# Optimization experiments

Measured on AMD Instinct MI355X. Metric: run time of the kernel, lower is better.

Reference implementation:

```python
import jax, jax.numpy as jnp
import numpy as np

EMBED_DIM = 128
NUM_HEADS = 4
HEAD_DIM = EMBED_DIM // NUM_HEADS
B, S = 2, 1024


def setup_inputs() -> dict:
    key = jax.random.key(0)
    ks = jax.random.split(key, 9)
    sc = 1.0 / np.sqrt(EMBED_DIM)
    x = jax.random.normal(ks[0], (B, S, EMBED_DIM), dtype=jnp.float32)
    # torch nn.Linear weights: (out_features, in_features)
    Wq = jax.random.uniform(ks[1], (EMBED_DIM, EMBED_DIM), jnp.float32, -sc, sc)
    bq = jax.random.uniform(ks[2], (EMBED_DIM,), jnp.float32, -sc, sc)
    Wk = jax.random.uniform(ks[3], (EMBED_DIM, EMBED_DIM), jnp.float32, -sc, sc)
    bk = jax.random.uniform(ks[4], (EMBED_DIM,), jnp.float32, -sc, sc)
    Wv = jax.random.uniform(ks[5], (EMBED_DIM, EMBED_DIM), jnp.float32, -sc, sc)
    bv = jax.random.uniform(ks[6], (EMBED_DIM,), jnp.float32, -sc, sc)
    Wo = jax.random.uniform(ks[7], (EMBED_DIM, EMBED_DIM), jnp.float32, -sc, sc)
    bo = jax.random.uniform(ks[8], (EMBED_DIM,), jnp.float32, -sc, sc)
    return {"x": x, "Wq": Wq, "bq": bq, "Wk": Wk, "bk": bk,
            "Wv": Wv, "bv": bv, "Wo": Wo, "bo": bo}


def _heads(y):
    # (B,S,E) -> (B,H,S,D)
    return y.reshape(B, S, NUM_HEADS, HEAD_DIM).transpose(0, 2, 1, 3)


def reference(x, Wq, bq, Wk, bk, Wv, bv, Wo, bo):
    q = _heads(x @ Wq.T + bq)  # (B,H,S,D)
    k = _heads(x @ Wk.T + bk)
    v = _heads(x @ Wv.T + bv)
    # ultrametric (Chebyshev / max-abs) distance: (B,H,S,S)
    dist = jnp.max(jnp.abs(q[:, :, :, None, :] - k[:, :, None, :, :]), axis=-1)
    attn = jax.nn.softmax(-dist, axis=-1)
    attended = jnp.einsum('bhst,bhtd->bhsd', attn, v)
    attended = attended.transpose(0, 2, 1, 3).reshape(B, S, EMBED_DIM)
    return attended @ Wo.T + bo
```

## Files before the change

kernel.cpp:

```cpp
#include <hip/hip_runtime.h>
#include <hip/hip_bf16.h>

#define B_ 2
#define S_ 1024
#define E_ 128
#define H_ 4
#define D_ 32
#define BHSD (B_ * H_ * S_ * D_)
#define LOG2E 1.44269504088896f

__global__ __launch_bounds__(128) void qkv_kernel(
    const float* __restrict__ x,
    const float* __restrict__ Wq, const float* __restrict__ bq,
    const float* __restrict__ Wk, const float* __restrict__ bk,
    const float* __restrict__ Wv, const float* __restrict__ bv,
    float* __restrict__ ws) {
  const int mat = blockIdx.y;
  const float* W    = (mat == 0) ? Wq : (mat == 1) ? Wk : Wv;
  const float* bias = (mat == 0) ? bq : (mat == 1) ? bk : bv;
  const float scale = (mat == 2) ? 1.0f : LOG2E;
  float* outbase = ws + (size_t)mat * BHSD;

  const int row0 = blockIdx.x * 8;
  const int t = threadIdx.x;

  __shared__ __align__(16) float xs[8 * E_];
  const float4* xg = (const float4*)(x + (size_t)row0 * E_);
  float4* xs4 = (float4*)xs;
  #pragma unroll
  for (int i = 0; i < 2; ++i) xs4[t + i * 128] = xg[t + i * 128];
  __syncthreads();

  const int col = t;
  const float4* W4 = (const float4*)(W + (size_t)col * E_);

  float acc[8];
  #pragma unroll
  for (int r = 0; r < 8; ++r) acc[r] = 0.f;

  #pragma unroll 4
  for (int c4 = 0; c4 < E_ / 4; ++c4) {
    float4 w = W4[c4];
    #pragma unroll
    for (int r = 0; r < 8; ++r) {
      float4 xv = xs4[r * (E_ / 4) + c4];
      acc[r] += xv.x * w.x + xv.y * w.y + xv.z * w.z + xv.w * w.w;
    }
  }

  const float bcol = bias[col];
  const int h = col >> 5, d = col & 31;
  #pragma unroll
  for (int r = 0; r < 8; ++r) {
    int row = row0 + r;
    int b = row >> 10, s = row & 1023;
    outbase[(((size_t)(b * H_ + h)) * S_ + s) * D_ + d] = (acc[r] + bcol) * scale;
  }
}

#define QSTRIDE 36
#define PSTRIDE 68

__global__ __launch_bounds__(256) void attn_kernel(
    const float* __restrict__ qg, const float* __restrict__ kg_,
    const float* __restrict__ vg,
    float* __restrict__ part_o, float* __restrict__ part_l) {
  __shared__ __align__(16) float Qs[64 * QSTRIDE];
  __shared__ __align__(16) float Ks[64 * QSTRIDE];
  __shared__ __align__(16) float Vs[64 * QSTRIDE];
  __shared__ __align__(16) float Ps[64 * PSTRIDE];

  const int bx = blockIdx.x;
  const int kc  = bx & 3;
  const int rtl = (bx >> 2) & 15;
  const int head = bx >> 6;
  const int t = threadIdx.x;
  const int w = t >> 6;
  const int lane = t & 63;
  const int rg = lane >> 3;
  const int kg = lane & 7;

  const float* qbase = qg  + (size_t)head * S_ * D_ + (size_t)rtl * 64 * D_;
  const float* kbase = kg_ + (size_t)head * S_ * D_ + (size_t)kc * 256 * D_;
  const float* vbase = vg  + (size_t)head * S_ * D_ + (size_t)kc * 256 * D_;

  {
    const float4* src = (const float4*)qbase;
    #pragma unroll
    for (int i = 0; i < 2; ++i) {
      int f = t + i * 256;
      int r = f >> 3, c4 = f & 7;
      *(float4*)(Qs + r * QSTRIDE + c4 * 4) = src[f];
    }
  }

  float O[8][4];
  #pragma unroll
  for (int i = 0; i < 8; ++i)
    #pragma unroll
    for (int c = 0; c < 4; ++c) O[i][c] = 0.f;
  float lrow[8];
  #pragma unroll
  for (int i = 0; i < 8; ++i) lrow[i] = 0.f;

  for (int it = 0; it < 4; ++it) {
    {
      const float4* ksrc = (const float4*)(kbase + (size_t)it * 64 * D_);
      const float4* vsrc = (const float4*)(vbase + (size_t)it * 64 * D_);
      #pragma unroll
      for (int i = 0; i < 2; ++i) {
        int f = t + i * 256;
        int r = f >> 3, c4 = f & 7;
        *(float4*)(Ks + r * QSTRIDE + c4 * 4) = ksrc[f];
        *(float4*)(Vs + r * QSTRIDE + c4 * 4) = vsrc[f];
      }
    }
    __syncthreads();

    float dist[8][2];
    #pragma unroll
    for (int i = 0; i < 8; ++i) { dist[i][0] = 0.f; dist[i][1] = 0.f; }

    #pragma unroll 2
    for (int c = 0; c < 8; ++c) {
      float4 qv[8];
      #pragma unroll
      for (int i = 0; i < 8; ++i)
        qv[i] = *(const float4*)(Qs + (rg + 8 * i) * QSTRIDE + c * 4);
      float4 kv[2];
      #pragma unroll
      for (int j = 0; j < 2; ++j)
        kv[j] = *(const float4*)(Ks + (w * 16 + kg + 8 * j) * QSTRIDE + c * 4);
      #pragma unroll
      for (int i = 0; i < 8; ++i) {
        #pragma unroll
        for (int j = 0; j < 2; ++j) {
          float m0 = fmaxf(fabsf(qv[i].x - kv[j].x), fabsf(qv[i].y - kv[j].y));
          float m1 = fmaxf(fabsf(qv[i].z - kv[j].z), fabsf(qv[i].w - kv[j].w));
          dist[i][j] = fmaxf(dist[i][j], fmaxf(m0, m1));
        }
      }
    }

    float pp[8][2];
    #pragma unroll
    for (int i = 0; i < 8; ++i) {
      #pragma unroll
      for (int j = 0; j < 2; ++j) {
        float p = exp2f(-dist[i][j]);
        pp[i][j] = p;
        lrow[i] += p;
      }
    }
    #pragma unroll
    for (int j = 0; j < 2; ++j) {
      float* dst = Ps + (w * 16 + kg + 8 * j) * PSTRIDE + rg * 8;
      *(float4*)(dst + 0) = make_float4(pp[0][j], pp[1][j], pp[2][j], pp[3][j]);
      *(float4*)(dst + 4) = make_float4(pp[4][j], pp[5][j], pp[6][j], pp[7][j]);
    }
    __syncthreads();

    const int tk0 = w * 16;
    #pragma unroll 4
    for (int u = 0; u < 16; ++u) {
      const int tk = tk0 + u;
      float4 pa = *(const float4*)(Ps + tk * PSTRIDE + rg * 8);
      float4 pb = *(const float4*)(Ps + tk * PSTRIDE + rg * 8 + 4);
      float4 vv = *(const float4*)(Vs + tk * QSTRIDE + kg * 4);
      O[0][0] = fmaf(pa.x, vv.x, O[0][0]); O[0][1] = fmaf(pa.x, vv.y, O[0][1]);
      O[0][2] = fmaf(pa.x, vv.z, O[0][2]); O[0][3] = fmaf(pa.x, vv.w, O[0][3]);
      O[1][0] = fmaf(pa.y, vv.x, O[1][0]); O[1][1] = fmaf(pa.y, vv.y, O[1][1]);
      O[1][2] = fmaf(pa.y, vv.z, O[1][2]); O[1][3] = fmaf(pa.y, vv.w, O[1][3]);
      O[2][0] = fmaf(pa.z, vv.x, O[2][0]); O[2][1] = fmaf(pa.z, vv.y, O[2][1]);
      O[2][2] = fmaf(pa.z, vv.z, O[2][2]); O[2][3] = fmaf(pa.z, vv.w, O[2][3]);
      O[3][0] = fmaf(pa.w, vv.x, O[3][0]); O[3][1] = fmaf(pa.w, vv.y, O[3][1]);
      O[3][2] = fmaf(pa.w, vv.z, O[3][2]); O[3][3] = fmaf(pa.w, vv.w, O[3][3]);
      O[4][0] = fmaf(pb.x, vv.x, O[4][0]); O[4][1] = fmaf(pb.x, vv.y, O[4][1]);
      O[4][2] = fmaf(pb.x, vv.z, O[4][2]); O[4][3] = fmaf(pb.x, vv.w, O[4][3]);
      O[5][0] = fmaf(pb.y, vv.x, O[5][0]); O[5][1] = fmaf(pb.y, vv.y, O[5][1]);
      O[5][2] = fmaf(pb.y, vv.z, O[5][2]); O[5][3] = fmaf(pb.y, vv.w, O[5][3]);
      O[6][0] = fmaf(pb.z, vv.x, O[6][0]); O[6][1] = fmaf(pb.z, vv.y, O[6][1]);
      O[6][2] = fmaf(pb.z, vv.z, O[6][2]); O[6][3] = fmaf(pb.z, vv.w, O[6][3]);
      O[7][0] = fmaf(pb.w, vv.x, O[7][0]); O[7][1] = fmaf(pb.w, vv.y, O[7][1]);
      O[7][2] = fmaf(pb.w, vv.z, O[7][2]); O[7][3] = fmaf(pb.w, vv.w, O[7][3]);
    }
    __syncthreads();
  }

  #pragma unroll
  for (int i = 0; i < 8; ++i) {
    lrow[i] += __shfl_xor(lrow[i], 1);
    lrow[i] += __shfl_xor(lrow[i], 2);
    lrow[i] += __shfl_xor(lrow[i], 4);
  }

  float* slbuf = Ps + 64 * 64;
  if (kg == 0) {
    #pragma unroll
    for (int i = 0; i < 8; ++i) slbuf[w * 64 + (rg + 8 * i)] = lrow[i];
  }
  if (w == 1) {
    #pragma unroll
    for (int i = 0; i < 8; ++i)
      *(float4*)(Ks + (rg + 8 * i) * QSTRIDE + kg * 4) =
          make_float4(O[i][0], O[i][1], O[i][2], O[i][3]);
  } else if (w == 2) {
    #pragma unroll
    for (int i = 0; i < 8; ++i)
      *(float4*)(Vs + (rg + 8 * i) * QSTRIDE + kg * 4) =
          make_float4(O[i][0], O[i][1], O[i][2], O[i][3]);
  } else if (w == 3) {
    #pragma unroll
    for (int i = 0; i < 8; ++i)
      *(float4*)(Qs + (rg + 8 * i) * QSTRIDE + kg * 4) =
          make_float4(O[i][0], O[i][1], O[i][2], O[i][3]);
  }
  __syncthreads();

  if (w == 0) {
    const size_t base = ((size_t)(head * 16 + rtl) * 4 + kc) * 64;
    #pragma unroll
    for (int i = 0; i < 8; ++i) {
      const int ar = rg + 8 * i;
      float4 a = *(const float4*)(Ks + ar * QSTRIDE + kg * 4);
      float4 b = *(const float4*)(Vs + ar * QSTRIDE + kg * 4);
      float4 c = *(const float4*)(Qs + ar * QSTRIDE + kg * 4);
      float4 r;
      r.x = O[i][0] + a.x + b.x + c.x;
      r.y = O[i][1] + a.y + b.y + c.y;
      r.z = O[i][2] + a.z + b.z + c.z;
      r.w = O[i][3] + a.w + b.w + c.w;
      *(float4*)(part_o + (base + ar) * 32 + kg * 4) = r;
    }
    if (kg == 0) {
      #pragma unroll
      for (int i = 0; i < 8; ++i) {
        const int ar = rg + 8 * i;
        part_l[base + ar] = slbuf[0 * 64 + ar] + slbuf[1 * 64 + ar] +
                            slbuf[2 * 64 + ar] + slbuf[3 * 64 + ar];
      }
    }
  }
}

__global__ __launch_bounds__(128) void out_kernel(
    const float* __restrict__ part_o, const float* __restrict__ part_l,
    const float* __restrict__ Wo, const float* __restrict__ bo,
    float* __restrict__ out) {
  const int row0 = blockIdx.x * 8;
  const int t = threadIdx.x;

  __shared__ __align__(16) float xs[8 * E_];

  const int e = t;
  const int h = e >> 5, d = e & 31;
  #pragma unroll
  for (int i = 0; i < 8; ++i) {
    const int r = row0 + i;
    const int b = r >> 10, s = r & 1023;
    const int rt = (b * H_ + h) * 16 + (s >> 6);
    const int lrow = s & 63;
    float acc = 0.f, lsum = 0.f;
    #pragma unroll
    for (int kc = 0; kc < 4; ++kc) {
      const size_t base = (size_t)(rt * 4 + kc) * 64 + lrow;
      acc  += part_o[base * 32 + d];
      lsum += part_l[base];
    }
    xs[i * E_ + e] = acc / lsum;
  }
  __syncthreads();

  const int col = t;
  const float4* W4 = (const float4*)(Wo + (size_t)col * E_);
  const float4* xs4 = (const float4*)xs;

  float acc[8];
  #pragma unroll
  for (int r = 0; r < 8; ++r) acc[r] = 0.f;

  #pragma unroll 4
  for (int c4 = 0; c4 < E_ / 4; ++c4) {
    float4 w = W4[c4];
    #pragma unroll
    for (int r = 0; r < 8; ++r) {
      float4 xv = xs4[r * (E_ / 4) + c4];
      acc[r] += xv.x * w.x + xv.y * w.y + xv.z * w.z + xv.w * w.w;
    }
  }

  const float bcol = bo[col];
  #pragma unroll
  for (int r = 0; r < 8; ++r)
    out[(size_t)(row0 + r) * E_ + col] = acc[r] + bcol;
}

extern "C" void kernel_launch(void* const* d_in, const int* in_sizes, int n_in,
                              void* d_out, int out_size, void* d_ws, size_t ws_size,
                              hipStream_t stream) {
  const float* x  = (const float*)d_in[0];
  const float* Wq = (const float*)d_in[1];
  const float* bq = (const float*)d_in[2];
  const float* Wk = (const float*)d_in[3];
  const float* bk = (const float*)d_in[4];
  const float* Wv = (const float*)d_in[5];
  const float* bv = (const float*)d_in[6];
  const float* Wo = (const float*)d_in[7];
  const float* bo = (const float*)d_in[8];
  float* ws  = (float*)d_ws;
  float* out = (float*)d_out;

  float* qd = ws;
  float* kd = ws + (size_t)BHSD;
  float* vd = ws + 2 * (size_t)BHSD;
  float* part_o = ws + 3 * (size_t)BHSD;
  float* part_l = part_o + (size_t)128 * 4 * 64 * 32;

  qkv_kernel<<<dim3((B_ * S_) / 8, 3), 128, 0, stream>>>(x, Wq, bq, Wk, bk, Wv, bv, ws);
  attn_kernel<<<dim3(512), 256, 0, stream>>>(qd, kd, vd, part_o, part_l);
  out_kernel<<<dim3((B_ * S_) / 8), 128, 0, stream>>>(part_o, part_l, Wo, bo, out);
}
```

Measured before the change: 50.67 us.

## Halve attention query tile to 32 rows and double the attention grid

Shrinks each attention block's query tile from 64 to 32 rows, so the grid grows to 1024 blocks. Per-thread accumulators, distances and the P buffer all shrink, and the partial-output indexing in the combine kernel is updated to match. It also drops the block-wide barrier between writing P and the P·V loop, since each wave only reads the P rows it wrote itself. More blocks and lower register and LDS use should improve occupancy, at the cost of loading each K/V tile twice as often and less register reuse of K per Q row.

```diff
diff --git a/kernel.cpp b/kernel.cpp
--- a/kernel.cpp
+++ b/kernel.cpp
@@ -59,49 +59,45 @@
 }
 
 #define QSTRIDE 36
-#define PSTRIDE 68
 
 __global__ __launch_bounds__(256) void attn_kernel(
     const float* __restrict__ qg, const float* __restrict__ kg_,
     const float* __restrict__ vg,
     float* __restrict__ part_o, float* __restrict__ part_l) {
-  __shared__ __align__(16) float Qs[64 * QSTRIDE];
+  __shared__ __align__(16) float Qs[32 * QSTRIDE];
   __shared__ __align__(16) float Ks[64 * QSTRIDE];
   __shared__ __align__(16) float Vs[64 * QSTRIDE];
-  __shared__ __align__(16) float Ps[64 * PSTRIDE];
+  __shared__ __align__(16) float Ps[64 * QSTRIDE];
 
   const int bx = blockIdx.x;
-  const int kc  = bx & 3;
-  const int rtl = (bx >> 2) & 15;
-  const int head = bx >> 6;
+  const int kc   = bx & 3;
+  const int rt   = bx >> 2;
+  const int head = rt >> 5;
+  const int rtl  = rt & 31;
   const int t = threadIdx.x;
   const int w = t >> 6;
   const int lane = t & 63;
   const int rg = lane >> 3;
   const int kg = lane & 7;
 
-  const float* qbase = qg  + (size_t)head * S_ * D_ + (size_t)rtl * 64 * D_;
+  const float* qbase = qg  + (size_t)head * S_ * D_ + (size_t)rtl * 32 * D_;
   const float* kbase = kg_ + (size_t)head * S_ * D_ + (size_t)kc * 256 * D_;
   const float* vbase = vg  + (size_t)head * S_ * D_ + (size_t)kc * 256 * D_;
 
   {
     const float4* src = (const float4*)qbase;
-    #pragma unroll
-    for (int i = 0; i < 2; ++i) {
-      int f = t + i * 256;
-      int r = f >> 3, c4 = f & 7;
-      *(float4*)(Qs + r * QSTRIDE + c4 * 4) = src[f];
-    }
-  }
-
-  float O[8][4];
-  #pragma unroll
-  for (int i = 0; i < 8; ++i)
+    int rr = t >> 3, c4 = t & 7;
+    *(float4*)(Qs + rr * QSTRIDE + c4 * 4) = src[t];
+  }
+
+  float O[4][4];
+  #pragma unroll
+  for (int i = 0; i < 4; ++i)
     #pragma unroll
     for (int c = 0; c < 4; ++c) O[i][c] = 0.f;
-  float lrow[8];
-  #pragma unroll
-  for (int i = 0; i < 8; ++i) lrow[i] = 0.f;
+  float lrow[4];
+  #pragma unroll
+  for (int i = 0; i < 4; ++i) lrow[i] = 0.f;
 
   for (int it = 0; it < 4; ++it) {
     {
@@ -110,29 +106,29 @@
       #pragma unroll
       for (int i = 0; i < 2; ++i) {
         int f = t + i * 256;
-        int r = f >> 3, c4 = f & 7;
-        *(float4*)(Ks + r * QSTRIDE + c4 * 4) = ksrc[f];
-        *(float4*)(Vs + r * QSTRIDE + c4 * 4) = vsrc[f];
+        int rr = f >> 3, c4 = f & 7;
+        *(float4*)(Ks + rr * QSTRIDE + c4 * 4) = ksrc[f];
+        *(float4*)(Vs + rr * QSTRIDE + c4 * 4) = vsrc[f];
       }
     }
     __syncthreads();
 
-    float dist[8][2];
-    #pragma unroll
-    for (int i = 0; i < 8; ++i) { dist[i][0] = 0.f; dist[i][1] = 0.f; }
-
-    #pragma unroll 2
+    float dist[4][2];
+    #pragma unroll
+    for (int i = 0; i < 4; ++i) { dist[i][0] = 0.f; dist[i][1] = 0.f; }
+
+    #pragma unroll
     for (int c = 0; c < 8; ++c) {
-      float4 qv[8];
-      #pragma unroll
-      for (int i = 0; i < 8; ++i)
+      float4 qv[4];
+      #pragma unroll
+      for (int i = 0; i < 4; ++i)
         qv[i] = *(const float4*)(Qs + (rg + 8 * i) * QSTRIDE + c * 4);
       float4 kv[2];
       #pragma unroll
       for (int j = 0; j < 2; ++j)
         kv[j] = *(const float4*)(Ks + (w * 16 + kg + 8 * j) * QSTRIDE + c * 4);
       #pragma unroll
-      for (int i = 0; i < 8; ++i) {
+      for (int i = 0; i < 4; ++i) {
         #pragma unroll
         for (int j = 0; j < 2; ++j) {
           float m0 = fmaxf(fabsf(qv[i].x - kv[j].x), fabsf(qv[i].y - kv[j].y));
@@ -142,9 +138,9 @@
       }
     }
 
-    float pp[8][2];
-    #pragma unroll
-    for (int i = 0; i < 8; ++i) {
+    float pp[4][2];
+    #pragma unroll
+    for (int i = 0; i < 4; ++i) {
       #pragma unroll
       for (int j = 0; j < 2; ++j) {
         float p = exp2f(-dist[i][j]);
@@ -154,18 +150,15 @@
     }
     #pragma unroll
     for (int j = 0; j < 2; ++j) {
-      float* dst = Ps + (w * 16 + kg + 8 * j) * PSTRIDE + rg * 8;
-      *(float4*)(dst + 0) = make_float4(pp[0][j], pp[1][j], pp[2][j], pp[3][j]);
-      *(float4*)(dst + 4) = make_float4(pp[4][j], pp[5][j], pp[6][j], pp[7][j]);
-    }
-    __syncthreads();
+      float* dst = Ps + (w * 16 + kg + 8 * j) * QSTRIDE + rg * 4;
+      *(float4*)dst = make_float4(pp[0][j], pp[1][j], pp[2][j], pp[3][j]);
+    }
 
     const int tk0 = w * 16;
     #pragma unroll 4
     for (int u = 0; u < 16; ++u) {
       const int tk = tk0 + u;
-      float4 pa = *(const float4*)(Ps + tk * PSTRIDE + rg * 8);
-      float4 pb = *(const float4*)(Ps + tk * PSTRIDE + rg * 8 + 4);
+      float4 pa = *(const float4*)(Ps + tk * QSTRIDE + rg * 4);
       float4 vv = *(const float4*)(Vs + tk * QSTRIDE + kg * 4);
       O[0][0] = fmaf(pa.x, vv.x, O[0][0]); O[0][1] = fmaf(pa.x, vv.y, O[0][1]);
       O[0][2] = fmaf(pa.x, vv.z, O[0][2]); O[0][3] = fmaf(pa.x, vv.w, O[0][3]);
@@ -175,56 +168,48 @@
       O[2][2] = fmaf(pa.z, vv.z, O[2][2]); O[2][3] = fmaf(pa.z, vv.w, O[2][3]);
       O[3][0] = fmaf(pa.w, vv.x, O[3][0]); O[3][1] = fmaf(pa.w, vv.y, O[3][1]);
       O[3][2] = fmaf(pa.w, vv.z, O[3][2]); O[3][3] = fmaf(pa.w, vv.w, O[3][3]);
-      O[4][0] = fmaf(pb.x, vv.x, O[4][0]); O[4][1] = fmaf(pb.x, vv.y, O[4][1]);
-      O[4][2] = fmaf(pb.x, vv.z, O[4][2]); O[4][3] = fmaf(pb.x, vv.w, O[4][3]);
-      O[5][0] = fmaf(pb.y, vv.x, O[5][0]); O[5][1] = fmaf(pb.y, vv.y, O[5][1]);
-      O[5][2] = fmaf(pb.y, vv.z, O[5][2]); O[5][3] = fmaf(pb.y, vv.w, O[5][3]);
-      O[6][0] = fmaf(pb.z, vv.x, O[6][0]); O[6][1] = fmaf(pb.z, vv.y, O[6][1]);
-      O[6][2] = fmaf(pb.z, vv.z, O[6][2]); O[6][3] = fmaf(pb.z, vv.w, O[6][3]);
-      O[7][0] = fmaf(pb.w, vv.x, O[7][0]); O[7][1] = fmaf(pb.w, vv.y, O[7][1]);
-      O[7][2] = fmaf(pb.w, vv.z, O[7][2]); O[7][3] = fmaf(pb.w, vv.w, O[7][3]);
     }
     __syncthreads();
   }
 
   #pragma unroll
-  for (int i = 0; i < 8; ++i) {
+  for (int i = 0; i < 4; ++i) {
     lrow[i] += __shfl_xor(lrow[i], 1);
     lrow[i] += __shfl_xor(lrow[i], 2);
     lrow[i] += __shfl_xor(lrow[i], 4);
   }
 
-  float* slbuf = Ps + 64 * 64;
+  float* slbuf = Ps;
   if (kg == 0) {
     #pragma unroll
-    for (int i = 0; i < 8; ++i) slbuf[w * 64 + (rg + 8 * i)] = lrow[i];
+    for (int i = 0; i < 4; ++i) slbuf[w * 32 + (rg + 8 * i)] = lrow[i];
   }
   if (w == 1) {
     #pragma unroll
-    for (int i = 0; i < 8; ++i)
+    for (int i = 0; i < 4; ++i)
       *(float4*)(Ks + (rg + 8 * i) * QSTRIDE + kg * 4) =
           make_float4(O[i][0], O[i][1], O[i][2], O[i][3]);
   } else if (w == 2) {
     #pragma unroll
-    for (int i = 0; i < 8; ++i)
+    for (int i = 0; i < 4; ++i)
+      *(float4*)(Ks + (32 + rg + 8 * i) * QSTRIDE + kg * 4) =
+          make_float4(O[i][0], O[i][1], O[i][2], O[i][3]);
+  } else if (w == 3) {
+    #pragma unroll
+    for (int i = 0; i < 4; ++i)
       *(float4*)(Vs + (rg + 8 * i) * QSTRIDE + kg * 4) =
           make_float4(O[i][0], O[i][1], O[i][2], O[i][3]);
-  } else if (w == 3) {
-    #pragma unroll
-    for (int i = 0; i < 8; ++i)
-      *(float4*)(Qs + (rg + 8 * i) * QSTRIDE + kg * 4) =
-          make_float4(O[i][0], O[i][1], O[i][2], O[i][3]);
   }
   __syncthreads();
 
   if (w == 0) {
-    const size_t base = ((size_t)(head * 16 + rtl) * 4 + kc) * 64;
-    #pragma unroll
-    for (int i = 0; i < 8; ++i) {
+    const size_t base = (size_t)(rt * 4 + kc) * 32;
+    #pragma unroll
+    for (int i = 0; i < 4; ++i) {
       const int ar = rg + 8 * i;
       float4 a = *(const float4*)(Ks + ar * QSTRIDE + kg * 4);
-      float4 b = *(const float4*)(Vs + ar * QSTRIDE + kg * 4);
-      float4 c = *(const float4*)(Qs + ar * QSTRIDE + kg * 4);
+      float4 b = *(const float4*)(Ks + (32 + ar) * QSTRIDE + kg * 4);
+      float4 c = *(const float4*)(Vs + ar * QSTRIDE + kg * 4);
       float4 r;
       r.x = O[i][0] + a.x + b.x + c.x;
       r.y = O[i][1] + a.y + b.y + c.y;
@@ -234,10 +219,10 @@
     }
     if (kg == 0) {
       #pragma unroll
-      for (int i = 0; i < 8; ++i) {
+      for (int i = 0; i < 4; ++i) {
         const int ar = rg + 8 * i;
-        part_l[base + ar] = slbuf[0 * 64 + ar] + slbuf[1 * 64 + ar] +
-                            slbuf[2 * 64 + ar] + slbuf[3 * 64 + ar];
+        part_l[base + ar] = slbuf[0 * 32 + ar] + slbuf[1 * 32 + ar] +
+                            slbuf[2 * 32 + ar] + slbuf[3 * 32 + ar];
       }
     }
   }
@@ -258,12 +243,12 @@
   for (int i = 0; i < 8; ++i) {
     const int r = row0 + i;
     const int b = r >> 10, s = r & 1023;
-    const int rt = (b * H_ + h) * 16 + (s >> 6);
-    const int lrow = s & 63;
+    const int rt = (b * H_ + h) * 32 + (s >> 5);
+    const int lrow = s & 31;
     float acc = 0.f, lsum = 0.f;
     #pragma unroll
     for (int kc = 0; kc < 4; ++kc) {
-      const size_t base = (size_t)(rt * 4 + kc) * 64 + lrow;
+      const size_t base = (size_t)(rt * 4 + kc) * 32 + lrow;
       acc  += part_o[base * 32 + d];
       lsum += part_l[base];
     }
@@ -314,9 +299,9 @@
   float* kd = ws + (size_t)BHSD;
   float* vd = ws + 2 * (size_t)BHSD;
   float* part_o = ws + 3 * (size_t)BHSD;
-  float* part_l = part_o + (size_t)128 * 4 * 64 * 32;
+  float* part_l = part_o + (size_t)256 * 4 * 32 * 32;
 
   qkv_kernel<<<dim3((B_ * S_) / 8, 3), 128, 0, stream>>>(x, Wq, bq, Wk, bk, Wv, bv, ws);
-  attn_kernel<<<dim3(512), 256, 0, stream>>>(qd, kd, vd, part_o, part_l);
+  attn_kernel<<<dim3(1024), 256, 0, stream>>>(qd, kd, vd, part_o, part_l);
   out_kernel<<<dim3((B_ * S_) / 8), 128, 0, stream>>>(part_o, part_l, Wo, bo, out);
 }
```

Measured after the change: 53.74 us. 6.1% more time.

## Double-buffer K/V tiles with register prefetch and drop the redundant barrier

Applied to the files above, without the earlier changes.

The attention kernel now loads the next K/V tile from global memory into registers before computing the current tile. It writes that tile into an alternate LDS buffer afterwards, so each iteration needs one barrier instead of two. The barrier between writing and reading P is removed because each wavefront reads only the P rows it wrote itself. Launch bounds now request two blocks per CU and the outer loop is fully unrolled. The cost is more LDS for the second K/V buffer and more registers held for the prefetched tile.

```diff
diff --git a/kernel.cpp b/kernel.cpp
--- a/kernel.cpp
+++ b/kernel.cpp
@@ -60,14 +60,15 @@
 
 #define QSTRIDE 36
 #define PSTRIDE 68
-
-__global__ __launch_bounds__(256) void attn_kernel(
+#define KBUF (64 * QSTRIDE)
+
+__global__ __launch_bounds__(256, 2) void attn_kernel(
     const float* __restrict__ qg, const float* __restrict__ kg_,
     const float* __restrict__ vg,
     float* __restrict__ part_o, float* __restrict__ part_l) {
   __shared__ __align__(16) float Qs[64 * QSTRIDE];
-  __shared__ __align__(16) float Ks[64 * QSTRIDE];
-  __shared__ __align__(16) float Vs[64 * QSTRIDE];
+  __shared__ __align__(16) float Ks[2 * KBUF];
+  __shared__ __align__(16) float Vs[2 * KBUF];
   __shared__ __align__(16) float Ps[64 * PSTRIDE];
 
   const int bx = blockIdx.x;
@@ -84,14 +85,23 @@
   const float* kbase = kg_ + (size_t)head * S_ * D_ + (size_t)kc * 256 * D_;
   const float* vbase = vg  + (size_t)head * S_ * D_ + (size_t)kc * 256 * D_;
 
+  const int rr0 = t >> 3, c40 = t & 7;
+  const int rr1 = (t + 256) >> 3, c41 = t & 7;
+
   {
-    const float4* src = (const float4*)qbase;
+    const float4* qsrc = (const float4*)qbase;
     #pragma unroll
     for (int i = 0; i < 2; ++i) {
       int f = t + i * 256;
-      int r = f >> 3, c4 = f & 7;
-      *(float4*)(Qs + r * QSTRIDE + c4 * 4) = src[f];
-    }
+      int rr = f >> 3, c4 = f & 7;
+      *(float4*)(Qs + rr * QSTRIDE + c4 * 4) = qsrc[f];
+    }
+    const float4* ksrc = (const float4*)kbase;
+    const float4* vsrc = (const float4*)vbase;
+    *(float4*)(Ks + rr0 * QSTRIDE + c40 * 4) = ksrc[t];
+    *(float4*)(Ks + rr1 * QSTRIDE + c41 * 4) = ksrc[t + 256];
+    *(float4*)(Vs + rr0 * QSTRIDE + c40 * 4) = vsrc[t];
+    *(float4*)(Vs + rr1 * QSTRIDE + c41 * 4) = vsrc[t + 256];
   }
 
   float O[8][4];
@@ -103,19 +113,20 @@
   #pragma unroll
   for (int i = 0; i < 8; ++i) lrow[i] = 0.f;
 
+  __syncthreads();
+
+  #pragma unroll
   for (int it = 0; it < 4; ++it) {
-    {
-      const float4* ksrc = (const float4*)(kbase + (size_t)it * 64 * D_);
-      const float4* vsrc = (const float4*)(vbase + (size_t)it * 64 * D_);
-      #pragma unroll
-      for (int i = 0; i < 2; ++i) {
-        int f = t + i * 256;
-        int r = f >> 3, c4 = f & 7;
-        *(float4*)(Ks + r * QSTRIDE + c4 * 4) = ksrc[f];
-        *(float4*)(Vs + r * QSTRIDE + c4 * 4) = vsrc[f];
-      }
-    }
-    __syncthreads();
+    float* Kc = Ks + (it & 1) * KBUF;
+    float* Vc = Vs + (it & 1) * KBUF;
+
+    float4 nk0, nk1, nv0, nv1;
+    if (it < 3) {
+      const float4* ksrc = (const float4*)(kbase + (size_t)(it + 1) * 64 * D_);
+      const float4* vsrc = (const float4*)(vbase + (size_t)(it + 1) * 64 * D_);
+      nk0 = ksrc[t]; nk1 = ksrc[t + 256];
+      nv0 = vsrc[t]; nv1 = vsrc[t + 256];
+    }
 
     float dist[8][2];
     #pragma unroll
@@ -130,7 +141,7 @@
       float4 kv[2];
       #pragma unroll
       for (int j = 0; j < 2; ++j)
-        kv[j] = *(const float4*)(Ks + (w * 16 + kg + 8 * j) * QSTRIDE + c * 4);
+        kv[j] = *(const float4*)(Kc + (w * 16 + kg + 8 * j) * QSTRIDE + c * 4);
       #pragma unroll
       for (int i = 0; i < 8; ++i) {
         #pragma unroll
@@ -158,7 +169,6 @@
       *(float4*)(dst + 0) = make_float4(pp[0][j], pp[1][j], pp[2][j], pp[3][j]);
       *(float4*)(dst + 4) = make_float4(pp[4][j], pp[5][j], pp[6][j], pp[7][j]);
     }
-    __syncthreads();
 
     const int tk0 = w * 16;
     #pragma unroll 4
@@ -166,7 +176,7 @@
       const int tk = tk0 + u;
       float4 pa = *(const float4*)(Ps + tk * PSTRIDE + rg * 8);
       float4 pb = *(const float4*)(Ps + tk * PSTRIDE + rg * 8 + 4);
-      float4 vv = *(const float4*)(Vs + tk * QSTRIDE + kg * 4);
+      float4 vv = *(const float4*)(Vc + tk * QSTRIDE + kg * 4);
       O[0][0] = fmaf(pa.x, vv.x, O[0][0]); O[0][1] = fmaf(pa.x, vv.y, O[0][1]);
       O[0][2] = fmaf(pa.x, vv.z, O[0][2]); O[0][3] = fmaf(pa.x, vv.w, O[0][3]);
       O[1][0] = fmaf(pa.y, vv.x, O[1][0]); O[1][1] = fmaf(pa.y, vv.y, O[1][1]);
@@ -184,6 +194,15 @@
       O[7][0] = fmaf(pb.w, vv.x, O[7][0]); O[7][1] = fmaf(pb.w, vv.y, O[7][1]);
       O[7][2] = fmaf(pb.w, vv.z, O[7][2]); O[7][3] = fmaf(pb.w, vv.w, O[7][3]);
     }
+
+    if (it < 3) {
+      float* Kn = Ks + ((it + 1) & 1) * KBUF;
+      float* Vn = Vs + ((it + 1) & 1) * KBUF;
+      *(float4*)(Kn + rr0 * QSTRIDE + c40 * 4) = nk0;
+      *(float4*)(Kn + rr1 * QSTRIDE + c41 * 4) = nk1;
+      *(float4*)(Vn + rr0 * QSTRIDE + c40 * 4) = nv0;
+      *(float4*)(Vn + rr1 * QSTRIDE + c41 * 4) = nv1;
+    }
     __syncthreads();
   }
 
```

Result: no change. 50.73 us (+0.1%).

## Retile attention so each wave owns 64 query rows and full key tiles

Applied to the files above, without the earlier changes.

The attention kernel now uses 128-thread blocks covering 128 query rows by 128 keys. Each wave computes an 8x8 register tile of distances over a full 64-key tile, so each query value loaded from shared memory is reused across more keys. Each wave also keeps its own private fp16 P buffer, which removes the cross-wave reduction through shared memory and one barrier per tile. The partial-sum layout grows to 8 key chunks, and out_kernel is updated to match. The trade-offs are fp16 rounding of the probabilities and higher register pressure from the dist[8][8] array, with launch bounds of (128,1).

```diff
diff --git a/kernel.cpp b/kernel.cpp
--- a/kernel.cpp
+++ b/kernel.cpp
@@ -1,5 +1,6 @@
 #include <hip/hip_runtime.h>
 #include <hip/hip_bf16.h>
+#include <hip/hip_fp16.h>
 
 #define B_ 2
 #define S_ 1024
@@ -58,21 +59,21 @@
   }
 }
 
-#define QSTRIDE 36
-#define PSTRIDE 68
-
-__global__ __launch_bounds__(256) void attn_kernel(
+#define STR 36
+#define PSTR 72
+
+__global__ __launch_bounds__(128, 1) void attn_kernel(
     const float* __restrict__ qg, const float* __restrict__ kg_,
     const float* __restrict__ vg,
     float* __restrict__ part_o, float* __restrict__ part_l) {
-  __shared__ __align__(16) float Qs[64 * QSTRIDE];
-  __shared__ __align__(16) float Ks[64 * QSTRIDE];
-  __shared__ __align__(16) float Vs[64 * QSTRIDE];
-  __shared__ __align__(16) float Ps[64 * PSTRIDE];
+  __shared__ __align__(16) float Qs[128 * STR];
+  __shared__ __align__(16) float Ks[64 * STR];
+  __shared__ __align__(16) float Vs[64 * STR];
+  __shared__ __align__(16) __half Ps[2 * 64 * PSTR];
 
   const int bx = blockIdx.x;
-  const int kc  = bx & 3;
-  const int rtl = (bx >> 2) & 15;
+  const int kc   = bx & 7;
+  const int rb   = (bx >> 3) & 7;
   const int head = bx >> 6;
   const int t = threadIdx.x;
   const int w = t >> 6;
@@ -80,17 +81,24 @@
   const int rg = lane >> 3;
   const int kg = lane & 7;
 
-  const float* qbase = qg  + (size_t)head * S_ * D_ + (size_t)rtl * 64 * D_;
-  const float* kbase = kg_ + (size_t)head * S_ * D_ + (size_t)kc * 256 * D_;
-  const float* vbase = vg  + (size_t)head * S_ * D_ + (size_t)kc * 256 * D_;
+  const float* qbase = qg  + (size_t)head * S_ * D_ + (size_t)rb * 128 * D_;
+  const float* kbase = kg_ + (size_t)head * S_ * D_ + (size_t)kc * 128 * D_;
+  const float* vbase = vg  + (size_t)head * S_ * D_ + (size_t)kc * 128 * D_;
 
   {
-    const float4* src = (const float4*)qbase;
-    #pragma unroll
-    for (int i = 0; i < 2; ++i) {
-      int f = t + i * 256;
-      int r = f >> 3, c4 = f & 7;
-      *(float4*)(Qs + r * QSTRIDE + c4 * 4) = src[f];
+    const float4* qsrc = (const float4*)qbase;
+    #pragma unroll
+    for (int i = 0; i < 8; ++i) {
+      int f = t + i * 128; int r = f >> 3, c = f & 7;
+      *(float4*)(Qs + r * STR + c * 4) = qsrc[f];
+    }
+    const float4* ksrc = (const float4*)kbase;
+    const float4* vsrc = (const float4*)vbase;
+    #pragma unroll
+    for (int i = 0; i < 4; ++i) {
+      int f = t + i * 128; int r = f >> 3, c = f & 7;
+      *(float4*)(Ks + r * STR + c * 4) = ksrc[f];
+      *(float4*)(Vs + r * STR + c * 4) = vsrc[f];
     }
   }
 
@@ -103,88 +111,92 @@
   #pragma unroll
   for (int i = 0; i < 8; ++i) lrow[i] = 0.f;
 
-  for (int it = 0; it < 4; ++it) {
-    {
-      const float4* ksrc = (const float4*)(kbase + (size_t)it * 64 * D_);
-      const float4* vsrc = (const float4*)(vbase + (size_t)it * 64 * D_);
-      #pragma unroll
-      for (int i = 0; i < 2; ++i) {
-        int f = t + i * 256;
-        int r = f >> 3, c4 = f & 7;
-        *(float4*)(Ks + r * QSTRIDE + c4 * 4) = ksrc[f];
-        *(float4*)(Vs + r * QSTRIDE + c4 * 4) = vsrc[f];
-      }
-    }
-    __syncthreads();
-
-    float dist[8][2];
-    #pragma unroll
-    for (int i = 0; i < 8; ++i) { dist[i][0] = 0.f; dist[i][1] = 0.f; }
-
-    #pragma unroll 2
+  __half* Psw = Ps + (size_t)w * 64 * PSTR;
+  const float* Qw = Qs + (size_t)(w * 64) * STR;
+
+  __syncthreads();
+
+  #pragma unroll
+  for (int it = 0; it < 2; ++it) {
+    float dist[8][8];
+    #pragma unroll
+    for (int i = 0; i < 8; ++i)
+      #pragma unroll
+      for (int j = 0; j < 8; ++j) dist[i][j] = 0.f;
+
+    #pragma unroll
     for (int c = 0; c < 8; ++c) {
       float4 qv[8];
       #pragma unroll
       for (int i = 0; i < 8; ++i)
-        qv[i] = *(const float4*)(Qs + (rg + 8 * i) * QSTRIDE + c * 4);
-      float4 kv[2];
-      #pragma unroll
-      for (int j = 0; j < 2; ++j)
-        kv[j] = *(const float4*)(Ks + (w * 16 + kg + 8 * j) * QSTRIDE + c * 4);
-      #pragma unroll
-      for (int i = 0; i < 8; ++i) {
+        qv[i] = *(const float4*)(Qw + (rg + 8 * i) * STR + c * 4);
+      #pragma unroll
+      for (int j = 0; j < 8; ++j) {
+        float4 kv = *(const float4*)(Ks + (kg + 8 * j) * STR + c * 4);
         #pragma unroll
-        for (int j = 0; j < 2; ++j) {
-          float m0 = fmaxf(fabsf(qv[i].x - kv[j].x), fabsf(qv[i].y - kv[j].y));
-          float m1 = fmaxf(fabsf(qv[i].z - kv[j].z), fabsf(qv[i].w - kv[j].w));
+        for (int i = 0; i < 8; ++i) {
+          float m0 = fmaxf(fabsf(qv[i].x - kv.x), fabsf(qv[i].y - kv.y));
+          float m1 = fmaxf(fabsf(qv[i].z - kv.z), fabsf(qv[i].w - kv.w));
           dist[i][j] = fmaxf(dist[i][j], fmaxf(m0, m1));
         }
       }
     }
 
-    float pp[8][2];
-    #pragma unroll
-    for (int i = 0; i < 8; ++i) {
-      #pragma unroll
-      for (int j = 0; j < 2; ++j) {
+    #pragma unroll
+    for (int j = 0; j < 8; ++j) {
+      #pragma unroll
+      for (int i = 0; i < 8; ++i) {
         float p = exp2f(-dist[i][j]);
-        pp[i][j] = p;
+        dist[i][j] = p;
         lrow[i] += p;
       }
-    }
-    #pragma unroll
-    for (int j = 0; j < 2; ++j) {
-      float* dst = Ps + (w * 16 + kg + 8 * j) * PSTRIDE + rg * 8;
-      *(float4*)(dst + 0) = make_float4(pp[0][j], pp[1][j], pp[2][j], pp[3][j]);
-      *(float4*)(dst + 4) = make_float4(pp[4][j], pp[5][j], pp[6][j], pp[7][j]);
-    }
+      __half2 hh[4];
+      hh[0] = __floats2half2_rn(dist[0][j], dist[1][j]);
+      hh[1] = __floats2half2_rn(dist[2][j], dist[3][j]);
+      hh[2] = __floats2half2_rn(dist[4][j], dist[5][j]);
+      hh[3] = __floats2half2_rn(dist[6][j], dist[7][j]);
+      *(uint4*)(Psw + (kg + 8 * j) * PSTR + rg * 8) = *(uint4*)hh;
+    }
+
+    #pragma unroll 8
+    for (int tk = 0; tk < 64; ++tk) {
+      uint4 pr = *(const uint4*)(Psw + tk * PSTR + rg * 8);
+      float4 vv = *(const float4*)(Vs + tk * STR + kg * 4);
+      __half2* ph = (__half2*)&pr;
+      float2 f0 = __half22float2(ph[0]);
+      float2 f1 = __half22float2(ph[1]);
+      float2 f2 = __half22float2(ph[2]);
+      float2 f3 = __half22float2(ph[3]);
+      O[0][0] = fmaf(f0.x, vv.x, O[0][0]); O[0][1] = fmaf(f0.x, vv.y, O[0][1]);
+      O[0][2] = fmaf(f0.x, vv.z, O[0][2]); O[0][3] = fmaf(f0.x, vv.w, O[0][3]);
+      O[1][0] = fmaf(f0.y, vv.x, O[1][0]); O[1][1] = fmaf(f0.y, vv.y, O[1][1]);
+      O[1][2] = fmaf(f0.y, vv.z, O[1][2]); O[1][3] = fmaf(f0.y, vv.w, O[1][3]);
+      O[2][0] = fmaf(f1.x, vv.x, O[2][0]); O[2][1] = fmaf(f1.x, vv.y, O[2][1]);
+      O[2][2] = fmaf(f1.x, vv.z, O[2][2]); O[2][3] = fmaf(f1.x, vv.w, O[2][3]);
+      O[3][0] = fmaf(f1.y, vv.x, O[3][0]); O[3][1] = fmaf(f1.y, vv.y, O[3][1]);
+      O[3][2] = fmaf(f1.y, vv.z, O[3][2]); O[3][3] = fmaf(f1.y, vv.w, O[3][3]);
+      O[4][0] = fmaf(f2.x, vv.x, O[4][0]); O[4][1] = fmaf(f2.x, vv.y, O[4][1]);
+      O[4][2] = fmaf(f2.x, vv.z, O[4][2]); O[4][3] = fmaf(f2.x, vv.w, O[4][3]);
+      O[5][0] = fmaf(f2.y, vv.x, O[5][0]); O[5][1] = fmaf(f2.y, vv.y, O[5][1]);
+      O[5][2] = fmaf(f2.y, vv.z, O[5][2]); O[5][3] = fmaf(f2.y, vv.w, O[5][3]);
+      O[6][0] = fmaf(f3.x, vv.x, O[6][0]); O[6][1] = fmaf(f3.x, vv.y, O[6][1]);
+      O[6][2] = fmaf(f3.x, vv.z, O[6][2]); O[6][3] = fmaf(f3.x, vv.w, O[6][3]);
+      O[7][0] = fmaf(f3.y, vv.x, O[7][0]); O[7][1] = fmaf(f3.y, vv.y, O[7][1]);
+      O[7][2] = fmaf(f3.y, vv.z, O[7][2]); O[7][3] = fmaf(f3.y, vv.w, O[7][3]);
+    }
+
     __syncthreads();
-
-    const int tk0 = w * 16;
-    #pragma unroll 4
-    for (int u = 0; u < 16; ++u) {
-      const int tk = tk0 + u;
-      float4 pa = *(const float4*)(Ps + tk * PSTRIDE + rg * 8);
-      float4 pb = *(const float4*)(Ps + tk * PSTRIDE + rg * 8 + 4);
-      float4 vv = *(const float4*)(Vs + tk * QSTRIDE + kg * 4);
-      O[0][0] = fmaf(pa.x, vv.x, O[0][0]); O[0][1] = fmaf(pa.x, vv.y, O[0][1]);
-      O[0][2] = fmaf(pa.x, vv.z, O[0][2]); O[0][3] = fmaf(pa.x, vv.w, O[0][3]);
-      O[1][0] = fmaf(pa.y, vv.x, O[1][0]); O[1][1] = fmaf(pa.y, vv.y, O[1][1]);
-      O[1][2] = fmaf(pa.y, vv.z, O[1][2]); O[1][3] = fmaf(pa.y, vv.w, O[1][3]);
-      O[2][0] = fmaf(pa.z, vv.x, O[2][0]); O[2][1] = fmaf(pa.z, vv.y, O[2][1]);
-      O[2][2] = fmaf(pa.z, vv.z, O[2][2]); O[2][3] = fmaf(pa.z, vv.w, O[2][3]);
-      O[3][0] = fmaf(pa.w, vv.x, O[3][0]); O[3][1] = fmaf(pa.w, vv.y, O[3][1]);
-      O[3][2] = fmaf(pa.w, vv.z, O[3][2]); O[3][3] = fmaf(pa.w, vv.w, O[3][3]);
-      O[4][0] = fmaf(pb.x, vv.x, O[4][0]); O[4][1] = fmaf(pb.x, vv.y, O[4][1]);
-      O[4][2] = fmaf(pb.x, vv.z, O[4][2]); O[4][3] = fmaf(pb.x, vv.w, O[4][3]);
-      O[5][0] = fmaf(pb.y, vv.x, O[5][0]); O[5][1] = fmaf(pb.y, vv.y, O[5][1]);
-      O[5][2] = fmaf(pb.y, vv.z, O[5][2]); O[5][3] = fmaf(pb.y, vv.w, O[5][3]);
-      O[6][0] = fmaf(pb.z, vv.x, O[6][0]); O[6][1] = fmaf(pb.z, vv.y, O[6][1]);
-      O[6][2] = fmaf(pb.z, vv.z, O[6][2]); O[6][3] = fmaf(pb.z, vv.w, O[6][3]);
-      O[7][0] = fmaf(pb.w, vv.x, O[7][0]); O[7][1] = fmaf(pb.w, vv.y, O[7][1]);
-      O[7][2] = fmaf(pb.w, vv.z, O[7][2]); O[7][3] = fmaf(pb.w, vv.w, O[7][3]);
-    }
-    __syncthreads();
+    if (it == 0) {
+      const float4* ksrc = (const float4*)(kbase + 64 * D_);
+      const float4* vsrc = (const float4*)(vbase + 64 * D_);
+      #pragma unroll
+      for (int i = 0; i < 4; ++i) {
+        int f = t + i * 128; int r = f >> 3, c = f & 7;
+        *(float4*)(Ks + r * STR + c * 4) = ksrc[f];
+        *(float4*)(Vs + r * STR + c * 4) = vsrc[f];
+      }
+      __syncthreads();
+    }
   }
 
   #pragma unroll
@@ -194,52 +206,18 @@
     lrow[i] += __shfl_xor(lrow[i], 4);
   }
 
-  float* slbuf = Ps + 64 * 64;
+  const int rt = head * 8 + rb;
+  const size_t base = ((size_t)(rt * 8 + kc)) * 128 + w * 64;
+  #pragma unroll
+  for (int i = 0; i < 8; ++i) {
+    const int ar = rg + 8 * i;
+    *(float4*)(part_o + (base + ar) * 32 + kg * 4) =
+        make_float4(O[i][0], O[i][1], O[i][2], O[i][3]);
+  }
   if (kg == 0) {
     #pragma unroll
-    for (int i = 0; i < 8; ++i) slbuf[w * 64 + (rg + 8 * i)] = lrow[i];
-  }
-  if (w == 1) {
-    #pragma unroll
     for (int i = 0; i < 8; ++i)
-      *(float4*)(Ks + (rg + 8 * i) * QSTRIDE + kg * 4) =
-          make_float4(O[i][0], O[i][1], O[i][2], O[i][3]);
-  } else if (w == 2) {
-    #pragma unroll
-    for (int i = 0; i < 8; ++i)
-      *(float4*)(Vs + (rg + 8 * i) * QSTRIDE + kg * 4) =
-          make_float4(O[i][0], O[i][1], O[i][2], O[i][3]);
-  } else if (w == 3) {
-    #pragma unroll
-    for (int i = 0; i < 8; ++i)
-      *(float4*)(Qs + (rg + 8 * i) * QSTRIDE + kg * 4) =
-          make_float4(O[i][0], O[i][1], O[i][2], O[i][3]);
-  }
-  __syncthreads();
-
-  if (w == 0) {
-    const size_t base = ((size_t)(head * 16 + rtl) * 4 + kc) * 64;
-    #pragma unroll
-    for (int i = 0; i < 8; ++i) {
-      const int ar = rg + 8 * i;
-      float4 a = *(const float4*)(Ks + ar * QSTRIDE + kg * 4);
-      float4 b = *(const float4*)(Vs + ar * QSTRIDE + kg * 4);
-      float4 c = *(const float4*)(Qs + ar * QSTRIDE + kg * 4);
-      float4 r;
-      r.x = O[i][0] + a.x + b.x + c.x;
-      r.y = O[i][1] + a.y + b.y + c.y;
-      r.z = O[i][2] + a.z + b.z + c.z;
-      r.w = O[i][3] + a.w + b.w + c.w;
-      *(float4*)(part_o + (base + ar) * 32 + kg * 4) = r;
-    }
-    if (kg == 0) {
-      #pragma unroll
-      for (int i = 0; i < 8; ++i) {
-        const int ar = rg + 8 * i;
-        part_l[base + ar] = slbuf[0 * 64 + ar] + slbuf[1 * 64 + ar] +
-                            slbuf[2 * 64 + ar] + slbuf[3 * 64 + ar];
-      }
-    }
+      part_l[base + rg + 8 * i] = lrow[i];
   }
 }
 
@@ -258,12 +236,12 @@
   for (int i = 0; i < 8; ++i) {
     const int r = row0 + i;
     const int b = r >> 10, s = r & 1023;
-    const int rt = (b * H_ + h) * 16 + (s >> 6);
-    const int lrow = s & 63;
+    const int rt = (b * H_ + h) * 8 + (s >> 7);
+    const int lrow = s & 127;
     float acc = 0.f, lsum = 0.f;
     #pragma unroll
-    for (int kc = 0; kc < 4; ++kc) {
-      const size_t base = (size_t)(rt * 4 + kc) * 64 + lrow;
+    for (int kc = 0; kc < 8; ++kc) {
+      const size_t base = ((size_t)(rt * 8 + kc)) * 128 + lrow;
       acc  += part_o[base * 32 + d];
       lsum += part_l[base];
     }
@@ -314,9 +292,9 @@
   float* kd = ws + (size_t)BHSD;
   float* vd = ws + 2 * (size_t)BHSD;
   float* part_o = ws + 3 * (size_t)BHSD;
-  float* part_l = part_o + (size_t)128 * 4 * 64 * 32;
+  float* part_l = part_o + (size_t)64 * 8 * 128 * 32;
 
   qkv_kernel<<<dim3((B_ * S_) / 8, 3), 128, 0, stream>>>(x, Wq, bq, Wk, bk, Wv, bv, ws);
-  attn_kernel<<<dim3(512), 256, 0, stream>>>(qd, kd, vd, part_o, part_l);
+  attn_kernel<<<dim3(512), 128, 0, stream>>>(qd, kd, vd, part_o, part_l);
   out_kernel<<<dim3((B_ * S_) / 8), 128, 0, stream>>>(part_o, part_l, Wo, bo, out);
 }
```

Measured after the change: 166.7 us. 3.29x slower.
